# Optimization experiments

Measured on AMD Instinct MI355X. Metric: run time of the kernel, lower is better.

The kernel has to match this reference:

```python
import jax, jax.numpy as jnp
import numpy as np

N = 30000      # nodes
E = 480000     # edges (before self loops)
DIN = 128      # dim_in
DH = 32        # dim_h (per-head out channels)
H1 = 8         # gat1 heads
H2 = 2         # gat2 heads
G = 64         # num graphs in batch
DOUT = 10      # dim_out
NEG_SLOPE = 0.2


def _glorot(key, shape):
    fan_in = shape[0]
    return jax.random.normal(key, shape, dtype=jnp.float32) / np.sqrt(fan_in)


def setup_inputs() -> dict:
    key = jax.random.key(0)
    ks = jax.random.split(key, 16)
    x = jax.random.normal(ks[0], (N, DIN), dtype=jnp.float32)
    edge_index = jax.random.randint(ks[1], (2, E), 0, N, dtype=jnp.int32)
    batch = jnp.sort(jax.random.randint(ks[2], (N,), 0, G, dtype=jnp.int32))
    # GATv2Conv layer 1: lin_l, lin_r (dim_in -> H1*DH), att (H1, DH), bias (H1*DH)
    W1l = _glorot(ks[3], (DIN, H1 * DH))
    W1r = _glorot(ks[4], (DIN, H1 * DH))
    a1 = _glorot(ks[5], (DH, H1)).T  # [H1, DH]
    b1 = jnp.zeros((H1 * DH,), dtype=jnp.float32)
    # GATv2Conv layer 2: (H1*DH -> H2*DH)
    W2l = _glorot(ks[6], (H1 * DH, H2 * DH))
    W2r = _glorot(ks[7], (H1 * DH, H2 * DH))
    a2 = _glorot(ks[8], (DH, H2)).T  # [H2, DH]
    b2 = jnp.zeros((H2 * DH,), dtype=jnp.float32)
    # MLP head: fc1(2*DH -> DH), fc2(DH -> DH//2), fc(DH//2 -> DOUT); stored [in,out]
    fc1_w = _glorot(ks[9], (2 * DH, DH)); fc1_b = jnp.zeros((DH,), jnp.float32)
    fc2_w = _glorot(ks[10], (DH, DH // 2)); fc2_b = jnp.zeros((DH // 2,), jnp.float32)
    fc_w = _glorot(ks[11], (DH // 2, DOUT)); fc_b = jnp.zeros((DOUT,), jnp.float32)
    return {"x": x, "edge_index": edge_index, "batch": batch,
            "W1l": W1l, "W1r": W1r, "a1": a1, "b1": b1,
            "W2l": W2l, "W2r": W2r, "a2": a2, "b2": b2,
            "fc1_w": fc1_w, "fc1_b": fc1_b, "fc2_w": fc2_w, "fc2_b": fc2_b,
            "fc_w": fc_w, "fc_b": fc_b}


def gatv2_conv(x, edge_index, Wl, Wr, att, bias, heads, dh, n):
    """PyG GATv2Conv: concat=True, add_self_loops=True, negative_slope=0.2."""
    src, dst = edge_index[0], edge_index[1]
    loop = jnp.arange(n, dtype=src.dtype)        # self loops (PyG default)
    src = jnp.concatenate([src, loop])
    dst = jnp.concatenate([dst, loop])
    xl = (x @ Wl).reshape(n, heads, dh)          # source transform
    xr = (x @ Wr).reshape(n, heads, dh)          # destination transform
    xj = xl[src]                                  # [Etot, H, dh] message features
    s = jax.nn.leaky_relu(xj + xr[dst], NEG_SLOPE)
    e = jnp.einsum('ehd,hd->eh', s, att)          # per-edge per-head score
    # segment softmax over incoming edges of each destination node
    m = jax.ops.segment_max(e, dst, num_segments=n)
    p = jnp.exp(e - m[dst])
    z = jax.ops.segment_sum(p, dst, num_segments=n)
    alpha = p / z[dst]                            # [Etot, H]
    out = jax.ops.segment_sum(xj * alpha[..., None], dst, num_segments=n)
    return out.reshape(n, heads * dh) + bias


def reference(x, edge_index, batch, W1l, W1r, a1, b1, W2l, W2r, a2, b2,
              fc1_w, fc1_b, fc2_w, fc2_b, fc_w, fc_b):
    h = gatv2_conv(x, edge_index, W1l, W1r, a1, b1, H1, DH, N)
    h = jax.nn.elu(h)
    h = gatv2_conv(h, edge_index, W2l, W2r, a2, b2, H2, DH, N)  # [N, 2*DH]
    # global_mean_pool
    sums = jax.ops.segment_sum(h, batch, num_segments=G)
    cnt = jax.ops.segment_sum(jnp.ones((N,), h.dtype), batch, num_segments=G)
    hg = sums / jnp.maximum(cnt, 1.0)[:, None]    # [G, 2*DH]
    x1 = jax.nn.relu(hg @ fc1_w + fc1_b)
    # dropout p=0.2 is identity in eval mode
    x2 = jax.nn.relu(x1 @ fc2_w + fc2_b)
    c = x2 @ fc_w + fc_b
    return (c, x2)
```

## Files before the change

### kernel.cpp

```cpp
#include <hip/hip_runtime.h>
#include <math.h>

#define DIN 128
#define DH  32
#define H1  8
#define H2  2
#define GNUM 64
#define DOUT 10
#define NEG_SLOPE 0.2f
#define SCAN_B 512

typedef __attribute__((ext_vector_type(8))) short sv8;
typedef __attribute__((ext_vector_type(4))) float fv4;

static __device__ __forceinline__ unsigned short f2bf(float f) {
    unsigned int u = __float_as_uint(f);
    unsigned int r = (u + 0x7fffu + ((u >> 16) & 1u)) >> 16;
    return (unsigned short)r;
}
static __device__ __forceinline__ float bf2f(unsigned short h) {
    return __uint_as_float(((unsigned int)h) << 16);
}


__global__ void k_prep(const float* __restrict__ x,
                       const float* __restrict__ W1l, const float* __restrict__ W1r,
                       const float* __restrict__ W2l, const float* __restrict__ W2r,
                       unsigned short* __restrict__ xgh, unsigned short* __restrict__ xgl,
                       short* __restrict__ B1th, short* __restrict__ B1tl,
                       short* __restrict__ B2th, short* __restrict__ B2tl,
                       int* __restrict__ zbase, int nz, int n) {
    int id = blockIdx.x * blockDim.x + threadIdx.x;
    if (id < nz) zbase[id] = 0;
    const int NX = n * 32;
    const int T1 = 512 * 128;
    const int T2 = 128 * 256;
    if (id < NX) {
        int m = id >> 5, j4 = id & 31;
        float4 v = *(const float4*)(x + (size_t)m * 128 + j4 * 4);
        unsigned short hx = f2bf(v.x), hy = f2bf(v.y), hz = f2bf(v.z), hw = f2bf(v.w);
        ushort4 hi; hi.x = hx; hi.y = hy; hi.z = hz; hi.w = hw;
        ushort4 lo;
        lo.x = f2bf(v.x - bf2f(hx)); lo.y = f2bf(v.y - bf2f(hy));
        lo.z = f2bf(v.z - bf2f(hz)); lo.w = f2bf(v.w - bf2f(hw));
        int R = m >> 4, r = m & 15;
        int C = j4 >> 3, q = (j4 >> 1) & 3, j = (j4 & 1) * 4;
        size_t o = ((size_t)(R * 4 + C) * 64 + q * 16 + r) * 8 + j;
        *(ushort4*)(xgh + o) = hi;
        *(ushort4*)(xgl + o) = lo;
    } else if (id < NX + T1) {
        int id1 = id - NX;
        int nn = id1 / 128, k = id1 - nn * 128;
        float v = (nn < 256) ? W1l[(size_t)k * 256 + nn] : W1r[(size_t)k * 256 + (nn - 256)];
        unsigned short h = f2bf(v);
        size_t o = (((size_t)(nn >> 4) * 4 + (k >> 5)) * 64 + ((k >> 3) & 3) * 16 + (nn & 15)) * 8 + (k & 7);
        B1th[o] = (short)h;
        B1tl[o] = (short)f2bf(v - bf2f(h));
    } else if (id < NX + T1 + T2) {
        int id2 = id - NX - T1;
        int nn = id2 / 256, k = id2 - nn * 256;
        float v = (nn < 64) ? W2l[(size_t)k * 64 + nn] : W2r[(size_t)k * 64 + (nn - 64)];
        unsigned short h = f2bf(v);
        size_t o = (((size_t)(nn >> 4) * 8 + (k >> 5)) * 64 + ((k >> 3) & 3) * 16 + (nn & 15)) * 8 + (k & 7);
        B2th[o] = (short)h;
        B2tl[o] = (short)f2bf(v - bf2f(h));
    }
}

__global__ void k_deg(const int* __restrict__ dst, int* __restrict__ deg, int E, int n) {
    int i = blockIdx.x * blockDim.x + threadIdx.x;
    if (i < E) {
        atomicAdd(&deg[dst[i]], 1);
    } else if (i < E + n) {
        atomicAdd(&deg[i - E], 1);
    }
}

__global__ __launch_bounds__(SCAN_B)
void k_scan_partial(const int* __restrict__ deg, int* __restrict__ bsum, int n) {
    int i = blockIdx.x * SCAN_B + threadIdx.x;
    int v = (i < n) ? deg[i] : 0;
    #pragma unroll
    for (int m = 32; m >= 1; m >>= 1) v += __shfl_xor(v, m);
    __shared__ int red[SCAN_B / 64];
    if ((threadIdx.x & 63) == 0) red[threadIdx.x >> 6] = v;
    __syncthreads();
    if (threadIdx.x == 0) {
        int s = 0;
        #pragma unroll
        for (int k = 0; k < SCAN_B / 64; ++k) s += red[k];
        bsum[blockIdx.x] = s;
    }
}

__global__ __launch_bounds__(SCAN_B)
void k_scan_apply(int* __restrict__ deg, int* __restrict__ cursor,
                  const int* __restrict__ bsum, int n, int nb) {
    __shared__ int buf[SCAN_B];
    __shared__ int pfx_s, tot_s;
    const int t = threadIdx.x, b = blockIdx.x;
    if (t < 64) {
        int v = (t < nb) ? bsum[t] : 0;
        int incl = v;
        #pragma unroll
        for (int o = 1; o < 64; o <<= 1) {
            int w = __shfl_up(incl, o);
            if (t >= o) incl += w;
        }
        int pfx = (b == 0) ? 0 : __shfl(incl, b - 1);
        int tot = __shfl(incl, nb - 1);
        if (t == 0) { pfx_s = pfx; tot_s = tot; }
    }
    int i = b * SCAN_B + t;
    int v = (i < n) ? deg[i] : 0;
    buf[t] = v;
    __syncthreads();
    for (int o = 1; o < SCAN_B; o <<= 1) {
        int a = (t >= o) ? buf[t - o] : 0;
        __syncthreads();
        buf[t] += a;
        __syncthreads();
    }
    int excl = buf[t] - v + pfx_s;
    if (i < n) { deg[i] = excl; cursor[i] = excl; }
    if (b == 0 && t == 0) deg[n] = tot_s;
}

__global__ void k_scatter(const int* __restrict__ src, const int* __restrict__ dst,
                          int* __restrict__ cursor, int* __restrict__ csr_src, int E, int n) {
    int i = blockIdx.x * blockDim.x + threadIdx.x;
    if (i < E) {
        int d = dst[i];
        int pos = atomicAdd(&cursor[d], 1);
        csr_src[pos] = src[i];
    } else if (i < E + n) {
        int v = i - E;
        int pos = atomicAdd(&cursor[v], 1);
        csr_src[pos] = v;
    }
}

__global__ __launch_bounds__(256, 2)
void k_gemm1(const unsigned short* __restrict__ Ah, const unsigned short* __restrict__ Al,
             const short* __restrict__ Bth, const short* __restrict__ Btl,
             unsigned short* __restrict__ C,
             int M, int Ntot) {
    __shared__ float smc[64 * 68];
    const int tid = threadIdx.x;
    const int lane = tid & 63;
    const int wid = tid >> 6;
    const int wm = wid & 1, wn = wid >> 1;
    const int m0 = blockIdx.x * 128;
    const int n0 = blockIdx.y * 128;
    const int l15 = lane & 15, q = lane >> 4;
    const int MR = (M >> 4) - 1;

    fv4 acc[4][4] = {};

    const unsigned short* ap[4];
    const unsigned short* alp[4];
    #pragma unroll
    for (int fm = 0; fm < 4; ++fm) {
        int R = (m0 >> 4) + wm * 4 + fm;
        if (R > MR) R = MR;
        ap[fm]  = Ah + ((size_t)R * 4 * 64 + lane) * 8;
        alp[fm] = Al + ((size_t)R * 4 * 64 + lane) * 8;
    }
    const short* bhp[4];
    const short* blp[4];
    #pragma unroll
    for (int fn = 0; fn < 4; ++fn) {
        int R = (n0 >> 4) + wn * 4 + fn;
        bhp[fn] = Bth + ((size_t)R * 4 * 64 + lane) * 8;
        blp[fn] = Btl + ((size_t)R * 4 * 64 + lane) * 8;
    }

    #pragma unroll
    for (int c = 0; c < 4; ++c) {
        const size_t co = (size_t)c * 512;
        sv8 ah[4], al[4], bh[4], bl[4];
        #pragma unroll
        for (int fn = 0; fn < 4; ++fn) {
            bh[fn] = *(const sv8*)(bhp[fn] + co);
            bl[fn] = *(const sv8*)(blp[fn] + co);
        }
        #pragma unroll
        for (int fm = 0; fm < 4; ++fm) {
            ah[fm] = *(const sv8*)(ap[fm] + co);
            al[fm] = *(const sv8*)(alp[fm] + co);
        }
        #pragma unroll
        for (int fm = 0; fm < 4; ++fm) {
            #pragma unroll
            for (int fn = 0; fn < 4; ++fn) {
                acc[fm][fn] = __builtin_amdgcn_mfma_f32_16x16x32_bf16(ah[fm], bh[fn], acc[fm][fn], 0, 0, 0);
                acc[fm][fn] = __builtin_amdgcn_mfma_f32_16x16x32_bf16(ah[fm], bl[fn], acc[fm][fn], 0, 0, 0);
                acc[fm][fn] = __builtin_amdgcn_mfma_f32_16x16x32_bf16(al[fm], bh[fn], acc[fm][fn], 0, 0, 0);
            }
        }
    }

    #pragma unroll
    for (int s = 0; s < 2; ++s) {
        #pragma unroll
        for (int cn = 0; cn < 2; ++cn) {
            __syncthreads();
            if (wm == s && wn == cn) {
                #pragma unroll
                for (int fm = 0; fm < 4; ++fm)
                    #pragma unroll
                    for (int fn = 0; fn < 4; ++fn)
                        #pragma unroll
                        for (int r = 0; r < 4; ++r)
                            smc[(fm * 16 + q * 4 + r) * 68 + fn * 16 + l15] = acc[fm][fn][r];
            }
            __syncthreads();
            int lr = tid >> 2;
            int grow = m0 + s * 64 + lr;
            if (grow < M) {
                #pragma unroll
                for (int k4 = 0; k4 < 4; ++k4) {
                    int jj = (tid & 3) + k4 * 4;
                    float4 vv = *(float4*)&smc[lr * 68 + jj * 4];
                    int gcol = n0 + cn * 64 + jj * 4;
                    ushort4 uu;
                    uu.x = f2bf(vv.x); uu.y = f2bf(vv.y);
                    uu.z = f2bf(vv.z); uu.w = f2bf(vv.w);
                    *(ushort4*)(C + (size_t)grow * Ntot + gcol) = uu;
                }
            }
        }
    }
}

__global__ __launch_bounds__(256, 2)
void k_gemm_bf(const unsigned short* __restrict__ A, const short* __restrict__ Bth,
               const short* __restrict__ Btl,
               unsigned short* __restrict__ C,
               int M, int Ntot) {
    __shared__ float smc[64 * 36];
    const int tid = threadIdx.x;
    const int lane = tid & 63;
    const int wid = tid >> 6;
    const int wm = wid & 1, wn = wid >> 1;
    const int m0 = blockIdx.x * 128;
    const int n0 = blockIdx.y * 64;
    const int l15 = lane & 15, q = lane >> 4;
    const int MR = (M >> 4) - 1;

    fv4 acc[4][2] = {};

    const unsigned short* ap[4];
    #pragma unroll
    for (int fm = 0; fm < 4; ++fm) {
        int R = (m0 >> 4) + wm * 4 + fm;
        if (R > MR) R = MR;
        ap[fm] = A + ((size_t)R * 8 * 64 + lane) * 8;
    }
    const short* bhp[2];
    const short* blp[2];
    #pragma unroll
    for (int fn = 0; fn < 2; ++fn) {
        int R = (n0 >> 4) + wn * 2 + fn;
        bhp[fn] = Bth + ((size_t)R * 8 * 64 + lane) * 8;
        blp[fn] = Btl + ((size_t)R * 8 * 64 + lane) * 8;
    }

    #pragma unroll 4
    for (int c = 0; c < 8; ++c) {
        const size_t co = (size_t)c * 512;
        sv8 ah[4], bh[2], bl[2];
        #pragma unroll
        for (int fn = 0; fn < 2; ++fn) {
            bh[fn] = *(const sv8*)(bhp[fn] + co);
            bl[fn] = *(const sv8*)(blp[fn] + co);
        }
        #pragma unroll
        for (int fm = 0; fm < 4; ++fm)
            ah[fm] = *(const sv8*)(ap[fm] + co);
        #pragma unroll
        for (int fm = 0; fm < 4; ++fm) {
            #pragma unroll
            for (int fn = 0; fn < 2; ++fn) {
                acc[fm][fn] = __builtin_amdgcn_mfma_f32_16x16x32_bf16(ah[fm], bh[fn], acc[fm][fn], 0, 0, 0);
                acc[fm][fn] = __builtin_amdgcn_mfma_f32_16x16x32_bf16(ah[fm], bl[fn], acc[fm][fn], 0, 0, 0);
            }
        }
    }

    #pragma unroll
    for (int s = 0; s < 2; ++s) {
        #pragma unroll
        for (int cn = 0; cn < 2; ++cn) {
            __syncthreads();
            if (wm == s && wn == cn) {
                #pragma unroll
                for (int fm = 0; fm < 4; ++fm)
                    #pragma unroll
                    for (int fn = 0; fn < 2; ++fn)
                        #pragma unroll
                        for (int r = 0; r < 4; ++r)
                            smc[(fm * 16 + q * 4 + r) * 36 + fn * 16 + l15] = acc[fm][fn][r];
            }
            __syncthreads();
            int lr = tid >> 2;
            int grow = m0 + s * 64 + lr;
            if (grow < M) {
                #pragma unroll
                for (int k4 = 0; k4 < 2; ++k4) {
                    int jj = (tid & 3) + k4 * 4;
                    float4 vv = *(float4*)&smc[lr * 36 + jj * 4];
                    int gcol = n0 + cn * 32 + jj * 4;
                    ushort4 uu;
                    uu.x = f2bf(vv.x); uu.y = f2bf(vv.y);
                    uu.z = f2bf(vv.z); uu.w = f2bf(vv.w);
                    *(ushort4*)(C + (size_t)grow * Ntot + gcol) = uu;
                }
            }
        }
    }
}

__global__ __launch_bounds__(64)
void k_edge1(const unsigned short* __restrict__ XLR,
             const int* __restrict__ offs, const int* __restrict__ csr,
             const float* __restrict__ att, const float* __restrict__ bias,
             unsigned short* __restrict__ out, int n) {
    const int lane = threadIdx.x;
    const int v = blockIdx.x;
    const int li = lane & 31;
    const int half = lane >> 5;
    const uint4* XL4 = (const uint4*)XLR;
    float av[8], xr[8];
    #pragma unroll
    for (int k = 0; k < 8; ++k) av[k] = att[li * 8 + k];
    {
        uint4 u = XL4[(size_t)v * 64 + 32 + li];
        xr[0] = __uint_as_float(u.x << 16);  xr[1] = __uint_as_float(u.x & 0xffff0000u);
        xr[2] = __uint_as_float(u.y << 16);  xr[3] = __uint_as_float(u.y & 0xffff0000u);
        xr[4] = __uint_as_float(u.z << 16);  xr[5] = __uint_as_float(u.z & 0xffff0000u);
        xr[6] = __uint_as_float(u.w << 16);  xr[7] = __uint_as_float(u.w & 0xffff0000u);
    }
    float z = 0.f;
    float acc[8] = {};
    const int e0 = offs[v], e1 = offs[v + 1];
    for (int j0 = e0; j0 < e1; j0 += 4) {
        #pragma unroll
        for (int p = 0; p < 2; ++p) {
            int j = j0 + p * 2 + half;
            bool valid = (j < e1);
            int jj = valid ? j : (e1 - 1);
            int src = csr[jj];
            uint4 u = XL4[(size_t)src * 64 + li];
            float f[8];
            f[0] = __uint_as_float(u.x << 16);  f[1] = __uint_as_float(u.x & 0xffff0000u);
            f[2] = __uint_as_float(u.y << 16);  f[3] = __uint_as_float(u.y & 0xffff0000u);
            f[4] = __uint_as_float(u.z << 16);  f[5] = __uint_as_float(u.z & 0xffff0000u);
            f[6] = __uint_as_float(u.w << 16);  f[7] = __uint_as_float(u.w & 0xffff0000u);
            float s1 = 0.f, s2 = 0.f;
            #pragma unroll
            for (int k = 0; k < 8; ++k) {
                float t = f[k] + xr[k];
                s1 = fmaf(t, av[k], s1);
                s2 = fmaf(fabsf(t), av[k], s2);
            }
            float s = fmaf(0.6f, s1, 0.4f * s2);
            s += __shfl_xor(s, 1);
            s += __shfl_xor(s, 2);
            float w = valid ? __expf(s) : 0.f;
            z += w;
            #pragma unroll
            for (int k = 0; k < 8; ++k) acc[k] = fmaf(w, f[k], acc[k]);
        }
    }
    z += __shfl_xor(z, 32);
    #pragma unroll
    for (int k = 0; k < 8; ++k) acc[k] += __shfl_xor(acc[k], 32);
    if (half == 0) {
        const float rz = 1.f / z;
        unsigned int o[4];
        #pragma unroll
        for (int k2 = 0; k2 < 4; ++k2) {
            float lo = fmaf(acc[k2 * 2 + 0], rz, bias[li * 8 + k2 * 2 + 0]);
            float hi = fmaf(acc[k2 * 2 + 1], rz, bias[li * 8 + k2 * 2 + 1]);
            lo = (lo > 0.f) ? lo : (__expf(lo) - 1.f);
            hi = (hi > 0.f) ? hi : (__expf(hi) - 1.f);
            o[k2] = (unsigned int)f2bf(lo) | ((unsigned int)f2bf(hi) << 16);
        }
        uint4 ov = { o[0], o[1], o[2], o[3] };
        size_t po = (((size_t)(v >> 4) * 8 + (li >> 2)) * 64 + (li & 3) * 16 + (v & 15)) * 8;
        *(uint4*)(out + po) = ov;
    }
}

__global__ __launch_bounds__(64)
void k_edge2(const unsigned short* __restrict__ XLR,
             const int* __restrict__ offs, const int* __restrict__ csr,
             const float* __restrict__ att, const float* __restrict__ bias,
             float* __restrict__ out, int n) {
    const int lane = threadIdx.x;
    const int v = blockIdx.x;
    const int li = lane & 7;
    const int slot = lane >> 3;
    const uint4* XL4 = (const uint4*)XLR;
    float av[8], xr[8];
    #pragma unroll
    for (int k = 0; k < 8; ++k) av[k] = att[li * 8 + k];
    {
        uint4 u = XL4[(size_t)v * 16 + 8 + li];
        xr[0] = __uint_as_float(u.x << 16);  xr[1] = __uint_as_float(u.x & 0xffff0000u);
        xr[2] = __uint_as_float(u.y << 16);  xr[3] = __uint_as_float(u.y & 0xffff0000u);
        xr[4] = __uint_as_float(u.z << 16);  xr[5] = __uint_as_float(u.z & 0xffff0000u);
        xr[6] = __uint_as_float(u.w << 16);  xr[7] = __uint_as_float(u.w & 0xffff0000u);
    }
    float z = 0.f;
    float acc[8] = {};
    const int e0 = offs[v], e1 = offs[v + 1];
    for (int j0 = e0; j0 < e1; j0 += 8) {
        int j = j0 + slot;
        bool valid = (j < e1);
        int jj = valid ? j : (e1 - 1);
        int src = csr[jj];
        uint4 u = XL4[(size_t)src * 16 + li];
        float f[8];
        f[0] = __uint_as_float(u.x << 16);  f[1] = __uint_as_float(u.x & 0xffff0000u);
        f[2] = __uint_as_float(u.y << 16);  f[3] = __uint_as_float(u.y & 0xffff0000u);
        f[4] = __uint_as_float(u.z << 16);  f[5] = __uint_as_float(u.z & 0xffff0000u);
        f[6] = __uint_as_float(u.w << 16);  f[7] = __uint_as_float(u.w & 0xffff0000u);
        float s1 = 0.f, s2 = 0.f;
        #pragma unroll
        for (int k = 0; k < 8; ++k) {
            float t = f[k] + xr[k];
            s1 = fmaf(t, av[k], s1);
            s2 = fmaf(fabsf(t), av[k], s2);
        }
        float s = fmaf(0.6f, s1, 0.4f * s2);
        s += __shfl_xor(s, 1);
        s += __shfl_xor(s, 2);
        float w = valid ? __expf(s) : 0.f;
        z += w;
        #pragma unroll
        for (int k = 0; k < 8; ++k) acc[k] = fmaf(w, f[k], acc[k]);
    }
    z += __shfl_xor(z, 8);  z += __shfl_xor(z, 16);  z += __shfl_xor(z, 32);
    #pragma unroll
    for (int k = 0; k < 8; ++k) {
        acc[k] += __shfl_xor(acc[k], 8);
        acc[k] += __shfl_xor(acc[k], 16);
        acc[k] += __shfl_xor(acc[k], 32);
    }
    if (slot == 0) {
        const float rz = 1.f / z;
        float o[8];
        #pragma unroll
        for (int k = 0; k < 8; ++k)
            o[k] = fmaf(acc[k], rz, bias[li * 8 + k]);
        float4 o0 = { o[0], o[1], o[2], o[3] };
        float4 o1 = { o[4], o[5], o[6], o[7] };
        *(float4*)(out + (size_t)v * 64 + li * 8 + 0) = o0;
        *(float4*)(out + (size_t)v * 64 + li * 8 + 4) = o1;
    }
}

__global__ __launch_bounds__(256)
void k_pool_mlp(const float* __restrict__ out2, const int* __restrict__ batch,
                const float* __restrict__ fc1w, const float* __restrict__ fc1b,
                const float* __restrict__ fc2w, const float* __restrict__ fc2b,
                const float* __restrict__ fcw,  const float* __restrict__ fcb,
                float* __restrict__ outc, float* __restrict__ outx2, int n) {
    const int g = blockIdx.x;
    const int t = threadIdx.x;
    const int lane = t & 63;
    const int w = t >> 6;
    __shared__ float red[4][64];
    __shared__ float hg_s[64];
    __shared__ float x1_s[32];
    __shared__ float x2_s[16];

    int lo = 0, hi = n;
    while (lo < hi) { int mid = (lo + hi) >> 1; if (batch[mid] < g) lo = mid + 1; else hi = mid; }
    const int start = lo;
    hi = n;
    while (lo < hi) { int mid = (lo + hi) >> 1; if (batch[mid] < g + 1) lo = mid + 1; else hi = mid; }
    const int end = lo;

    float s = 0.f;
    for (int v = start + w; v < end; v += 4)
        s += out2[(size_t)v * 64 + lane];
    red[w][lane] = s;
    __syncthreads();
    if (w == 0) {
        float tot = red[0][lane] + red[1][lane] + red[2][lane] + red[3][lane];
        float cnt = fmaxf((float)(end - start), 1.0f);
        hg_s[lane] = tot / cnt;
    }
    __syncthreads();
    if (t < 32) {
        float a = fc1b[t];
        #pragma unroll
        for (int k = 0; k < 64; ++k) a = fmaf(hg_s[k], fc1w[k * 32 + t], a);
        x1_s[t] = fmaxf(a, 0.f);
    }
    __syncthreads();
    if (t < 16) {
        float a = fc2b[t];
        #pragma unroll
        for (int k = 0; k < 32; ++k) a = fmaf(x1_s[k], fc2w[k * 16 + t], a);
        x2_s[t] = fmaxf(a, 0.f);
    }
    __syncthreads();
    if (t < DOUT) {
        float a = fcb[t];
        #pragma unroll
        for (int k = 0; k < 16; ++k) a = fmaf(x2_s[k], fcw[k * 10 + t], a);
        outc[g * DOUT + t] = a;
    }
    if (t < 16) outx2[g * 16 + t] = x2_s[t];
}

extern "C" void kernel_launch(void* const* d_in, const int* in_sizes, int n_in,
                              void* d_out, int out_size, void* d_ws, size_t ws_size,
                              hipStream_t stream) {
    const float* x    = (const float*)d_in[0];
    const int*   ei   = (const int*)d_in[1];
    const int*   batch= (const int*)d_in[2];
    const float* W1l  = (const float*)d_in[3];
    const float* W1r  = (const float*)d_in[4];
    const float* a1   = (const float*)d_in[5];
    const float* b1   = (const float*)d_in[6];
    const float* W2l  = (const float*)d_in[7];
    const float* W2r  = (const float*)d_in[8];
    const float* a2   = (const float*)d_in[9];
    const float* b2   = (const float*)d_in[10];
    const float* fc1w = (const float*)d_in[11];
    const float* fc1b = (const float*)d_in[12];
    const float* fc2w = (const float*)d_in[13];
    const float* fc2b = (const float*)d_in[14];
    const float* fcw  = (const float*)d_in[15];
    const float* fcb  = (const float*)d_in[16];

    const int N = in_sizes[2];
    const int E = in_sizes[1] / 2;
    const int ET = E + N;
    const int* esrc = ei;
    const int* edst = ei + E;
    const int NB = (N + SCAN_B - 1) / SCAN_B;

    char* ws = (char*)d_ws;
    size_t off = 0;
    unsigned short* xlr1b = (unsigned short*)(ws + off); off += (size_t)N * 512 * 2;
    unsigned short* h1b  = (unsigned short*)(ws + off);  off += (size_t)N * 256 * 2;
    float* out2 = (float*)(ws + off);            off += (size_t)N * 64 * 4;
    int*   deg   = (int*)(ws + off);             off += ((size_t)(N + 1) * 4 + 255) & ~255ull;
    int*   cursor= (int*)(ws + off);             off += ((size_t)N * 4 + 255) & ~255ull;
    int*   csr   = (int*)(ws + off);             off += ((size_t)ET * 4 + 255) & ~255ull;
    int*   bsum  = (int*)(ws + off);             off += ((size_t)(NB + 1) * 4 + 255) & ~255ull;
    short* B1th  = (short*)(ws + off);           off += (size_t)512 * 128 * 2;
    short* B1tl  = (short*)(ws + off);           off += (size_t)512 * 128 * 2;
    short* B2th  = (short*)(ws + off);           off += (size_t)128 * 256 * 2;
    short* B2tl  = (short*)(ws + off);           off += (size_t)128 * 256 * 2;
    unsigned short* xgh = (unsigned short*)(ws + off); off += (size_t)N * 128 * 2;
    unsigned short* xgl = (unsigned short*)(ws + off); off += (size_t)N * 128 * 2;
    unsigned short* xlr2b = xlr1b;
    (void)ws_size; (void)n_in; (void)out_size;

    float* outc  = (float*)d_out;
    float* outx2 = (float*)d_out + GNUM * DOUT;

    const int prep_tot = N * 32 + 512 * 128 + 128 * 256;
    k_prep<<<(prep_tot + 255) / 256, 256, 0, stream>>>(
        x, W1l, W1r, W2l, W2r, xgh, xgl, B1th, B1tl, B2th, B2tl, deg, N + 1, N);

    int tb = 256;
    int gb = (ET + tb - 1) / tb;
    k_deg<<<gb, tb, 0, stream>>>(edst, deg, E, N);
    k_scan_partial<<<NB, SCAN_B, 0, stream>>>(deg, bsum, N);
    k_scan_apply<<<NB, SCAN_B, 0, stream>>>(deg, cursor, bsum, N, NB);
    k_scatter<<<gb, tb, 0, stream>>>(esrc, edst, cursor, csr, E, N);

    dim3 g1((N + 127) / 128, 4);
    k_gemm1<<<g1, 256, 0, stream>>>(xgh, xgl, B1th, B1tl, xlr1b, N, 512);

    k_edge1<<<N, 64, 0, stream>>>(xlr1b, deg, csr, a1, b1, h1b, N);

    dim3 g2((N + 127) / 128, 2);
    k_gemm_bf<<<g2, 256, 0, stream>>>(h1b, B2th, B2tl, xlr2b, N, 128);

    k_edge2<<<N, 64, 0, stream>>>(xlr2b, deg, csr, a2, b2, out2, N);

    k_pool_mlp<<<GNUM, 256, 0, stream>>>(out2, batch, fc1w, fc1b, fc2w, fc2b,
                                         fcw, fcb, outc, outx2, N);
}
```

Measured before the change: 282.2 us.

## Pack four nodes per block in edge kernels, use exp2 and packed bf16 converts

Each edge kernel now runs four destination nodes per 256-thread block, one wave per node, instead of one 64-thread block per node. This cuts block-launch and scheduling overhead for the 30000 tiny blocks. The attention vector is pre-scaled by log2(e) so the per-edge softmax weight can use exp2f instead of __expf. The scalar software bf16 rounding is replaced with the packed v_cvt_pk_bf16_f32 instruction in the GEMM epilogues and the edge1 output. That instruction needs hardware support on the target, and its rounding may differ slightly from the manual round-to-nearest-even.

```diff
diff --git a/kernel.cpp b/kernel.cpp
--- a/kernel.cpp
+++ b/kernel.cpp
@@ -9,6 +9,7 @@
 #define DOUT 10
 #define NEG_SLOPE 0.2f
 #define SCAN_B 512
+#define LOG2E 1.4426950408889634f
 
 typedef __attribute__((ext_vector_type(8))) short sv8;
 typedef __attribute__((ext_vector_type(4))) float fv4;
@@ -20,6 +21,11 @@
 }
 static __device__ __forceinline__ float bf2f(unsigned short h) {
     return __uint_as_float(((unsigned int)h) << 16);
+}
+static __device__ __forceinline__ unsigned int cvtpk(float lo, float hi) {
+    unsigned int r;
+    asm("v_cvt_pk_bf16_f32 %0, %1, %2" : "=v"(r) : "v"(lo), "v"(hi));
+    return r;
 }
 
 
@@ -223,10 +229,8 @@
                     int jj = (tid & 3) + k4 * 4;
                     float4 vv = *(float4*)&smc[lr * 68 + jj * 4];
                     int gcol = n0 + cn * 64 + jj * 4;
-                    ushort4 uu;
-                    uu.x = f2bf(vv.x); uu.y = f2bf(vv.y);
-                    uu.z = f2bf(vv.z); uu.w = f2bf(vv.w);
-                    *(ushort4*)(C + (size_t)grow * Ntot + gcol) = uu;
+                    uint2 uu = { cvtpk(vv.x, vv.y), cvtpk(vv.z, vv.w) };
+                    *(uint2*)(C + (size_t)grow * Ntot + gcol) = uu;
                 }
             }
         }
@@ -311,29 +315,29 @@
                     int jj = (tid & 3) + k4 * 4;
                     float4 vv = *(float4*)&smc[lr * 36 + jj * 4];
                     int gcol = n0 + cn * 32 + jj * 4;
-                    ushort4 uu;
-                    uu.x = f2bf(vv.x); uu.y = f2bf(vv.y);
-                    uu.z = f2bf(vv.z); uu.w = f2bf(vv.w);
-                    *(ushort4*)(C + (size_t)grow * Ntot + gcol) = uu;
+                    uint2 uu = { cvtpk(vv.x, vv.y), cvtpk(vv.z, vv.w) };
+                    *(uint2*)(C + (size_t)grow * Ntot + gcol) = uu;
                 }
             }
         }
     }
 }
 
-__global__ __launch_bounds__(64)
+__global__ __launch_bounds__(256)
 void k_edge1(const unsigned short* __restrict__ XLR,
              const int* __restrict__ offs, const int* __restrict__ csr,
              const float* __restrict__ att, const float* __restrict__ bias,
              unsigned short* __restrict__ out, int n) {
-    const int lane = threadIdx.x;
-    const int v = blockIdx.x;
+    const int tid = threadIdx.x;
+    const int lane = tid & 63;
+    const int v = blockIdx.x * 4 + (tid >> 6);
+    if (v >= n) return;
     const int li = lane & 31;
     const int half = lane >> 5;
     const uint4* XL4 = (const uint4*)XLR;
     float av[8], xr[8];
     #pragma unroll
-    for (int k = 0; k < 8; ++k) av[k] = att[li * 8 + k];
+    for (int k = 0; k < 8; ++k) av[k] = att[li * 8 + k] * LOG2E;
     {
         uint4 u = XL4[(size_t)v * 64 + 32 + li];
         xr[0] = __uint_as_float(u.x << 16);  xr[1] = __uint_as_float(u.x & 0xffff0000u);
@@ -367,7 +371,7 @@
             float s = fmaf(0.6f, s1, 0.4f * s2);
             s += __shfl_xor(s, 1);
             s += __shfl_xor(s, 2);
-            float w = valid ? __expf(s) : 0.f;
+            float w = valid ? exp2f(s) : 0.f;
             z += w;
             #pragma unroll
             for (int k = 0; k < 8; ++k) acc[k] = fmaf(w, f[k], acc[k]);
@@ -385,7 +389,7 @@
             float hi = fmaf(acc[k2 * 2 + 1], rz, bias[li * 8 + k2 * 2 + 1]);
             lo = (lo > 0.f) ? lo : (__expf(lo) - 1.f);
             hi = (hi > 0.f) ? hi : (__expf(hi) - 1.f);
-            o[k2] = (unsigned int)f2bf(lo) | ((unsigned int)f2bf(hi) << 16);
+            o[k2] = cvtpk(lo, hi);
         }
         uint4 ov = { o[0], o[1], o[2], o[3] };
         size_t po = (((size_t)(v >> 4) * 8 + (li >> 2)) * 64 + (li & 3) * 16 + (v & 15)) * 8;
@@ -393,19 +397,21 @@
     }
 }
 
-__global__ __launch_bounds__(64)
+__global__ __launch_bounds__(256)
 void k_edge2(const unsigned short* __restrict__ XLR,
              const int* __restrict__ offs, const int* __restrict__ csr,
              const float* __restrict__ att, const float* __restrict__ bias,
              float* __restrict__ out, int n) {
-    const int lane = threadIdx.x;
-    const int v = blockIdx.x;
+    const int tid = threadIdx.x;
+    const int lane = tid & 63;
+    const int v = blockIdx.x * 4 + (tid >> 6);
+    if (v >= n) return;
     const int li = lane & 7;
     const int slot = lane >> 3;
     const uint4* XL4 = (const uint4*)XLR;
     float av[8], xr[8];
     #pragma unroll
-    for (int k = 0; k < 8; ++k) av[k] = att[li * 8 + k];
+    for (int k = 0; k < 8; ++k) av[k] = att[li * 8 + k] * LOG2E;
     {
         uint4 u = XL4[(size_t)v * 16 + 8 + li];
         xr[0] = __uint_as_float(u.x << 16);  xr[1] = __uint_as_float(u.x & 0xffff0000u);
@@ -437,7 +443,7 @@
         float s = fmaf(0.6f, s1, 0.4f * s2);
         s += __shfl_xor(s, 1);
         s += __shfl_xor(s, 2);
-        float w = valid ? __expf(s) : 0.f;
+        float w = valid ? exp2f(s) : 0.f;
         z += w;
         #pragma unroll
         for (int k = 0; k < 8; ++k) acc[k] = fmaf(w, f[k], acc[k]);
@@ -581,12 +587,12 @@
     dim3 g1((N + 127) / 128, 4);
     k_gemm1<<<g1, 256, 0, stream>>>(xgh, xgl, B1th, B1tl, xlr1b, N, 512);
 
-    k_edge1<<<N, 64, 0, stream>>>(xlr1b, deg, csr, a1, b1, h1b, N);
+    k_edge1<<<(N + 3) / 4, 256, 0, stream>>>(xlr1b, deg, csr, a1, b1, h1b, N);
 
     dim3 g2((N + 127) / 128, 2);
     k_gemm_bf<<<g2, 256, 0, stream>>>(h1b, B2th, B2tl, xlr2b, N, 128);
 
-    k_edge2<<<N, 64, 0, stream>>>(xlr2b, deg, csr, a2, b2, out2, N);
+    k_edge2<<<(N + 3) / 4, 256, 0, stream>>>(xlr2b, deg, csr, a2, b2, out2, N);
 
     k_pool_mlp<<<GNUM, 256, 0, stream>>>(out2, batch, fc1w, fc1b, fc2w, fc2b,
                                          fcw, fcb, outc, outx2, N);
```

New measurement: 278.3 us (median of 2 runs). About the same (-1.4%).
